# Kernel optimization log

Measured on AMD Instinct MI355X. Metric: run time of the kernel, lower is better.

Reference implementation:

```python
import jax, jax.numpy as jnp
import numpy as np
from jax import lax


def _gru_layer(x_seq, W, U, b, units):
    """Keras GRU (reset_after=True, gate order [z, r, h]) with activation=relu.
    x_seq: (B, T, F). Returns (ys (B,T,units), h_last (B,units))."""
    b_in, b_rec = b[0], b[1]                      # each (3*units,)
    # Precompute all input projections once: (B, T, 3*units)
    x_proj = jnp.einsum('btf,fj->btj', x_seq, W) + b_in
    B = x_seq.shape[0]
    h0 = jnp.zeros((B, units), dtype=x_seq.dtype)

    def step(h, xp_t):
        rec = h @ U + b_rec                        # (B, 3*units)
        zr = jax.nn.sigmoid(xp_t[:, :2 * units] + rec[:, :2 * units])
        z, r = zr[:, :units], zr[:, units:]
        hh = jax.nn.relu(xp_t[:, 2 * units:] + r * rec[:, 2 * units:])
        h_new = z * h + (1.0 - z) * hh
        return h_new, h_new

    h_last, ys = lax.scan(step, h0, jnp.swapaxes(x_proj, 0, 1))  # scan over T
    return jnp.swapaxes(ys, 0, 1), h_last


def setup_inputs() -> dict:
    key = jax.random.key(0)
    ks = jax.random.split(key, 6)
    B, T, F, U1, U2 = 64, 2048, 15, 256, 256
    s = lambda fan_in: 1.0 / np.sqrt(fan_in)
    return {
        'input_data': jax.random.normal(ks[0], (B, T, F), dtype=jnp.float32),
        'W1': jax.random.normal(ks[1], (F, 3 * U1), dtype=jnp.float32) * s(F),
        'U1': jax.random.normal(ks[2], (U1, 3 * U1), dtype=jnp.float32) * s(U1),
        'b1': jnp.zeros((2, 3 * U1), dtype=jnp.float32),
        'W2': jax.random.normal(ks[3], (U1, 3 * U2), dtype=jnp.float32) * s(U1),
        'U2': jax.random.normal(ks[4], (U2, 3 * U2), dtype=jnp.float32) * s(U2),
        'b2': jnp.zeros((2, 3 * U2), dtype=jnp.float32),
    }


def reference(input_data, W1, U1, b1, W2, U2, b2):
    u1 = U1.shape[0]
    u2 = U2.shape[0]
    seq1, state1 = _gru_layer(input_data, W1, U1, b1, u1)  # gru1: return_sequences + state
    seq2, state2 = _gru_layer(seq1, W2, U2, b2, u2)        # gru2: last output + state
    x = seq2[:, -1, :]                                      # last output (== state2)
    return (x, state1, state2)
```

## Files before the change

kernel.cpp:

```cpp
#include <hip/hip_runtime.h>

#define BB 64
#define TT 2048
#define FF 15
#define UU 256
#define N3 768

typedef _Float16 half8 __attribute__((ext_vector_type(8)));
typedef float f32x4 __attribute__((ext_vector_type(4)));

__device__ float g_seq1[BB * TT * UU];
__device__ float g_xp[(size_t)BB * TT * N3];
__device__ uint4 g_U1p[48 * 8 * 64];
__device__ uint4 g_U2p[48 * 8 * 64];
__device__ uint4 g_W2p[48 * 8 * 64];

__global__ __launch_bounds__(256) void prep_upk(const float* __restrict__ U,
                                                unsigned* __restrict__ Up) {
    int idx = blockIdx.x * 256 + threadIdx.x;
    int d = idx & 3, l = (idx >> 2) & 63, kt = (idx >> 8) & 7, nt = idx >> 11;
    int row = kt * 32 + ((l >> 4) << 3) + 2 * d;
    int col = nt * 16 + (l & 15);
    unsigned short lo = __builtin_bit_cast(unsigned short, (_Float16)U[row * N3 + col]);
    unsigned short hi = __builtin_bit_cast(unsigned short, (_Float16)U[(row + 1) * N3 + col]);
    Up[idx] = (unsigned)lo | ((unsigned)hi << 16);
}

__global__ __launch_bounds__(256) void gemm_k15(
    const float* __restrict__ x, const float* __restrict__ W1,
    const float* __restrict__ bin, float* __restrict__ C) {
    __shared__ float xr[8][FF];
    const int m0 = blockIdx.x * 8;
    const int j  = blockIdx.y * 256 + threadIdx.x;
    if (threadIdx.x < 8 * FF) {
        int r = threadIdx.x / FF, k = threadIdx.x - r * FF;
        xr[r][k] = x[(size_t)(m0 + r) * FF + k];
    }
    __syncthreads();
    float wv[FF];
#pragma unroll
    for (int k = 0; k < FF; k++) wv[k] = W1[k * N3 + j];
    const float bj = bin[j];
#pragma unroll
    for (int r = 0; r < 8; r++) {
        float a = bj;
#pragma unroll
        for (int k = 0; k < FF; k++) a += xr[r][k] * wv[k];
        C[(size_t)(m0 + r) * N3 + j] = a;
    }
}

__global__ __launch_bounds__(512) void gemm_xp_mfma(
    const float* __restrict__ A, const uint4* __restrict__ Wp,
    const float* __restrict__ bin, float* __restrict__ C) {
    const int tid = threadIdx.x, w = tid >> 6, lane = tid & 63;
    const int mt = w >> 1;
    const int nb = (w & 1) * 24;
    const int arow = blockIdx.x * 64 + mt * 16 + (lane & 15);
    const int ko   = (lane >> 4) * 8;

    f32x4 acc[24] = {};
    const float* ap = A + (size_t)arow * 256 + ko;

#pragma unroll
    for (int kt = 0; kt < 8; kt++) {
        float4 p0 = *(const float4*)(ap + kt * 32);
        float4 p1 = *(const float4*)(ap + kt * 32 + 4);
        half8 av;
        av[0] = (_Float16)p0.x; av[1] = (_Float16)p0.y;
        av[2] = (_Float16)p0.z; av[3] = (_Float16)p0.w;
        av[4] = (_Float16)p1.x; av[5] = (_Float16)p1.y;
        av[6] = (_Float16)p1.z; av[7] = (_Float16)p1.w;
        const uint4* wp = Wp + (size_t)(nb * 8 + kt) * 64 + lane;
#pragma unroll
        for (int n = 0; n < 24; n++) {
            half8 bf = __builtin_bit_cast(half8, wp[(size_t)n * 8 * 64]);
            acc[n] = __builtin_amdgcn_mfma_f32_16x16x32_f16(av, bf, acc[n], 0, 0, 0);
        }
    }
    const int rbase = blockIdx.x * 64 + mt * 16 + (lane >> 4) * 4;
#pragma unroll
    for (int n = 0; n < 24; n++) {
        int col = (nb + n) * 16 + (lane & 15);
        float bv = bin[col];
#pragma unroll
        for (int d = 0; d < 4; d++)
            C[(size_t)(rbase + d) * N3 + col] = acc[n][d] + bv;
    }
}

__global__ __launch_bounds__(512) __attribute__((amdgpu_waves_per_eu(2, 2)))
void gru_mfma2(const uint4* __restrict__ Up, const float* __restrict__ brec,
               const float* __restrict__ xp, float* __restrict__ seq_out,
               float* __restrict__ state_out, float* __restrict__ extra_out) {
    const int b = blockIdx.x, tid = threadIdx.x;
    const int w = tid >> 6, lane = tid & 63;
    const int l15 = lane & 15;
    const int uA = 32 * w + l15, uB = uA + 16;

    __shared__ __align__(16) _Float16 h2s[2][UU];

    const int tz = 2 * w, tr = 16 + 2 * w, th = 32 + 2 * w;
    half8 ub[48];
#pragma unroll
    for (int kt = 0; kt < 8; kt++) {
        ub[0 * 8 + kt] = __builtin_bit_cast(half8, Up[((tz + 0) * 8 + kt) * 64 + lane]);
        ub[1 * 8 + kt] = __builtin_bit_cast(half8, Up[((tz + 1) * 8 + kt) * 64 + lane]);
        ub[2 * 8 + kt] = __builtin_bit_cast(half8, Up[((tr + 0) * 8 + kt) * 64 + lane]);
        ub[3 * 8 + kt] = __builtin_bit_cast(half8, Up[((tr + 1) * 8 + kt) * 64 + lane]);
        ub[4 * 8 + kt] = __builtin_bit_cast(half8, Up[((th + 0) * 8 + kt) * 64 + lane]);
        ub[5 * 8 + kt] = __builtin_bit_cast(half8, Up[((th + 1) * 8 + kt) * 64 + lane]);
    }
    const float brzA = brec[uA], brrA = brec[uA + UU], brhA = brec[uA + 2 * UU];
    const float brzB = brec[uB], brrB = brec[uB + UU], brhB = brec[uB + 2 * UU];

    if (tid < 128) ((unsigned*)h2s[0])[tid] = 0u;
    float hA = 0.f, hB = 0.f;
    __syncthreads();

    const float* __restrict__ xpb = xp + (size_t)b * TT * N3;
    float xzA = xpb[uA], xrA = xpb[uA + UU], xhA = xpb[uA + 2 * UU];
    float xzB = xpb[uB], xrB = xpb[uB + UU], xhB = xpb[uB + 2 * UU];

    const int arow = (lane >> 4) << 3;

    for (int t = 0; t < TT; t++) {
        const float* xn = xpb + (size_t)(t + 1 < TT ? t + 1 : t) * N3;
        float xzAn = xn[uA], xrAn = xn[uA + UU], xhAn = xn[uA + 2 * UU];
        float xzBn = xn[uB], xrBn = xn[uB + UU], xhBn = xn[uB + 2 * UU];

        const _Float16* hcur = h2s[t & 1];
        f32x4 a0 = {0.f, 0.f, 0.f, 0.f}, a1 = a0, a2 = a0, a3 = a0, a4 = a0, a5 = a0;
#pragma unroll
        for (int kt = 0; kt < 8; kt++) {
            half8 av = *(const half8*)&hcur[kt * 32 + arow];
            a0 = __builtin_amdgcn_mfma_f32_16x16x32_f16(av, ub[0 * 8 + kt], a0, 0, 0, 0);
            a1 = __builtin_amdgcn_mfma_f32_16x16x32_f16(av, ub[1 * 8 + kt], a1, 0, 0, 0);
            a2 = __builtin_amdgcn_mfma_f32_16x16x32_f16(av, ub[2 * 8 + kt], a2, 0, 0, 0);
            a3 = __builtin_amdgcn_mfma_f32_16x16x32_f16(av, ub[3 * 8 + kt], a3, 0, 0, 0);
            a4 = __builtin_amdgcn_mfma_f32_16x16x32_f16(av, ub[4 * 8 + kt], a4, 0, 0, 0);
            a5 = __builtin_amdgcn_mfma_f32_16x16x32_f16(av, ub[5 * 8 + kt], a5, 0, 0, 0);
        }

        float zA = 1.f / (1.f + __expf(-(xzA + a0[0] + brzA)));
        float zB = 1.f / (1.f + __expf(-(xzB + a1[0] + brzB)));
        float rA = 1.f / (1.f + __expf(-(xrA + a2[0] + brrA)));
        float rB = 1.f / (1.f + __expf(-(xrB + a3[0] + brrB)));
        float hhA = xhA + rA * (a4[0] + brhA); hhA = hhA > 0.f ? hhA : 0.f;
        float hhB = xhB + rB * (a5[0] + brhB); hhB = hhB > 0.f ? hhB : 0.f;
        hA = zA * hA + (1.f - zA) * hhA;
        hB = zB * hB + (1.f - zB) * hhB;

        _Float16* hnxt = h2s[(t + 1) & 1];
        if (lane < 32) {
            int   u  = (lane < 16) ? uA : uB;
            float hv = (lane < 16) ? hA : hB;
            hnxt[u] = (_Float16)hv;
            if (seq_out)
                seq_out[(size_t)b * TT * UU + (size_t)t * UU + u] = hv;
        }
        __syncthreads();
        xzA = xzAn; xrA = xrAn; xhA = xhAn;
        xzB = xzBn; xrB = xrBn; xhB = xhBn;
    }

    if (lane < 32) {
        int   u  = (lane < 16) ? uA : uB;
        float hv = (lane < 16) ? hA : hB;
        state_out[b * UU + u] = hv;
        if (extra_out) extra_out[b * UU + u] = hv;
    }
}

extern "C" void kernel_launch(void* const* d_in, const int* in_sizes, int n_in,
                              void* d_out, int out_size, void* d_ws, size_t ws_size,
                              hipStream_t stream) {
    const float* x  = (const float*)d_in[0];
    const float* W1 = (const float*)d_in[1];
    const float* U1 = (const float*)d_in[2];
    const float* b1 = (const float*)d_in[3];
    const float* W2 = (const float*)d_in[4];
    const float* U2 = (const float*)d_in[5];
    const float* b2 = (const float*)d_in[6];
    float* out = (float*)d_out;

    uint4* U1p; hipGetSymbolAddress((void**)&U1p, HIP_SYMBOL(g_U1p));
    uint4* U2p; hipGetSymbolAddress((void**)&U2p, HIP_SYMBOL(g_U2p));
    uint4* W2p; hipGetSymbolAddress((void**)&W2p, HIP_SYMBOL(g_W2p));
    float* seq1; hipGetSymbolAddress((void**)&seq1, HIP_SYMBOL(g_seq1));
    float* xp;   hipGetSymbolAddress((void**)&xp,   HIP_SYMBOL(g_xp));

    prep_upk<<<384, 256, 0, stream>>>(U1, (unsigned*)U1p);
    prep_upk<<<384, 256, 0, stream>>>(U2, (unsigned*)U2p);
    prep_upk<<<384, 256, 0, stream>>>(W2, (unsigned*)W2p);

    gemm_k15<<<dim3(BB * TT / 8, 3), 256, 0, stream>>>(x, W1, b1, xp);
    gru_mfma2<<<BB, 512, 0, stream>>>(U1p, b1 + N3, xp, seq1, out + BB * UU, nullptr);

    gemm_xp_mfma<<<BB * TT / 64, 512, 0, stream>>>(seq1, W2p, b2, xp);
    gru_mfma2<<<BB, 512, 0, stream>>>(U2p, b2 + N3, xp, nullptr, out + 2 * BB * UU, out);
}
```

Measured before the change: 5.026 ms.

## Store seq1 and input projections in fp16 and reorder recurrent MFMAs

The intermediate buffers for the layer-1 output sequence and the input projections now hold fp16 instead of fp32. This halves the HBM traffic of the projection GEMMs and of the per-step xp loads in the recurrent kernels. The recurrent step also preloads all eight h fragments from shared memory before issuing the MFMAs, and computes the r/h gate chains ahead of the z gate so that the dependent math can start sooner. The cost is extra rounding of the projections and of seq1, which may reduce accuracy over the 2048 steps.

```diff
diff --git a/kernel.cpp b/kernel.cpp
--- a/kernel.cpp
+++ b/kernel.cpp
@@ -9,8 +9,8 @@
 typedef _Float16 half8 __attribute__((ext_vector_type(8)));
 typedef float f32x4 __attribute__((ext_vector_type(4)));
 
-__device__ float g_seq1[BB * TT * UU];
-__device__ float g_xp[(size_t)BB * TT * N3];
+__device__ _Float16 g_seq1[BB * TT * UU];
+__device__ _Float16 g_xp[(size_t)BB * TT * N3];
 __device__ uint4 g_U1p[48 * 8 * 64];
 __device__ uint4 g_U2p[48 * 8 * 64];
 __device__ uint4 g_W2p[48 * 8 * 64];
@@ -28,7 +28,7 @@
 
 __global__ __launch_bounds__(256) void gemm_k15(
     const float* __restrict__ x, const float* __restrict__ W1,
-    const float* __restrict__ bin, float* __restrict__ C) {
+    const float* __restrict__ bin, _Float16* __restrict__ C) {
     __shared__ float xr[8][FF];
     const int m0 = blockIdx.x * 8;
     const int j  = blockIdx.y * 256 + threadIdx.x;
@@ -46,13 +46,13 @@
         float a = bj;
 #pragma unroll
         for (int k = 0; k < FF; k++) a += xr[r][k] * wv[k];
-        C[(size_t)(m0 + r) * N3 + j] = a;
+        C[(size_t)(m0 + r) * N3 + j] = (_Float16)a;
     }
 }
 
 __global__ __launch_bounds__(512) void gemm_xp_mfma(
-    const float* __restrict__ A, const uint4* __restrict__ Wp,
-    const float* __restrict__ bin, float* __restrict__ C) {
+    const _Float16* __restrict__ A, const uint4* __restrict__ Wp,
+    const float* __restrict__ bin, _Float16* __restrict__ C) {
     const int tid = threadIdx.x, w = tid >> 6, lane = tid & 63;
     const int mt = w >> 1;
     const int nb = (w & 1) * 24;
@@ -60,17 +60,11 @@
     const int ko   = (lane >> 4) * 8;
 
     f32x4 acc[24] = {};
-    const float* ap = A + (size_t)arow * 256 + ko;
+    const _Float16* ap = A + (size_t)arow * 256 + ko;
 
 #pragma unroll
     for (int kt = 0; kt < 8; kt++) {
-        float4 p0 = *(const float4*)(ap + kt * 32);
-        float4 p1 = *(const float4*)(ap + kt * 32 + 4);
-        half8 av;
-        av[0] = (_Float16)p0.x; av[1] = (_Float16)p0.y;
-        av[2] = (_Float16)p0.z; av[3] = (_Float16)p0.w;
-        av[4] = (_Float16)p1.x; av[5] = (_Float16)p1.y;
-        av[6] = (_Float16)p1.z; av[7] = (_Float16)p1.w;
+        half8 av = *(const half8*)(ap + kt * 32);
         const uint4* wp = Wp + (size_t)(nb * 8 + kt) * 64 + lane;
 #pragma unroll
         for (int n = 0; n < 24; n++) {
@@ -85,13 +79,13 @@
         float bv = bin[col];
 #pragma unroll
         for (int d = 0; d < 4; d++)
-            C[(size_t)(rbase + d) * N3 + col] = acc[n][d] + bv;
+            C[(size_t)(rbase + d) * N3 + col] = (_Float16)(acc[n][d] + bv);
     }
 }
 
 __global__ __launch_bounds__(512) __attribute__((amdgpu_waves_per_eu(2, 2)))
 void gru_mfma2(const uint4* __restrict__ Up, const float* __restrict__ brec,
-               const float* __restrict__ xp, float* __restrict__ seq_out,
+               const _Float16* __restrict__ xp, _Float16* __restrict__ seq_out,
                float* __restrict__ state_out, float* __restrict__ extra_out) {
     const int b = blockIdx.x, tid = threadIdx.x;
     const int w = tid >> 6, lane = tid & 63;
@@ -118,36 +112,46 @@
     float hA = 0.f, hB = 0.f;
     __syncthreads();
 
-    const float* __restrict__ xpb = xp + (size_t)b * TT * N3;
-    float xzA = xpb[uA], xrA = xpb[uA + UU], xhA = xpb[uA + 2 * UU];
-    float xzB = xpb[uB], xrB = xpb[uB + UU], xhB = xpb[uB + 2 * UU];
+    const _Float16* __restrict__ xpb = xp + (size_t)b * TT * N3;
+    float xzA = (float)xpb[uA], xrA = (float)xpb[uA + UU], xhA = (float)xpb[uA + 2 * UU];
+    float xzB = (float)xpb[uB], xrB = (float)xpb[uB + UU], xhB = (float)xpb[uB + 2 * UU];
 
     const int arow = (lane >> 4) << 3;
+    const f32x4 kZ = {0.f, 0.f, 0.f, 0.f};
 
     for (int t = 0; t < TT; t++) {
-        const float* xn = xpb + (size_t)(t + 1 < TT ? t + 1 : t) * N3;
-        float xzAn = xn[uA], xrAn = xn[uA + UU], xhAn = xn[uA + 2 * UU];
-        float xzBn = xn[uB], xrBn = xn[uB + UU], xhBn = xn[uB + 2 * UU];
+        const _Float16* xn = xpb + (size_t)(t + 1 < TT ? t + 1 : t) * N3;
+        float xzAn = (float)xn[uA], xrAn = (float)xn[uA + UU], xhAn = (float)xn[uA + 2 * UU];
+        float xzBn = (float)xn[uB], xrBn = (float)xn[uB + UU], xhBn = (float)xn[uB + 2 * UU];
 
         const _Float16* hcur = h2s[t & 1];
-        f32x4 a0 = {0.f, 0.f, 0.f, 0.f}, a1 = a0, a2 = a0, a3 = a0, a4 = a0, a5 = a0;
-#pragma unroll
-        for (int kt = 0; kt < 8; kt++) {
-            half8 av = *(const half8*)&hcur[kt * 32 + arow];
-            a0 = __builtin_amdgcn_mfma_f32_16x16x32_f16(av, ub[0 * 8 + kt], a0, 0, 0, 0);
-            a1 = __builtin_amdgcn_mfma_f32_16x16x32_f16(av, ub[1 * 8 + kt], a1, 0, 0, 0);
-            a2 = __builtin_amdgcn_mfma_f32_16x16x32_f16(av, ub[2 * 8 + kt], a2, 0, 0, 0);
-            a3 = __builtin_amdgcn_mfma_f32_16x16x32_f16(av, ub[3 * 8 + kt], a3, 0, 0, 0);
-            a4 = __builtin_amdgcn_mfma_f32_16x16x32_f16(av, ub[4 * 8 + kt], a4, 0, 0, 0);
-            a5 = __builtin_amdgcn_mfma_f32_16x16x32_f16(av, ub[5 * 8 + kt], a5, 0, 0, 0);
+        half8 av[8];
+#pragma unroll
+        for (int kt = 0; kt < 8; kt++)
+            av[kt] = *(const half8*)&hcur[kt * 32 + arow];
+
+        f32x4 a2 = __builtin_amdgcn_mfma_f32_16x16x32_f16(av[0], ub[2 * 8], kZ, 0, 0, 0);
+        f32x4 a3 = __builtin_amdgcn_mfma_f32_16x16x32_f16(av[0], ub[3 * 8], kZ, 0, 0, 0);
+        f32x4 a4 = __builtin_amdgcn_mfma_f32_16x16x32_f16(av[0], ub[4 * 8], kZ, 0, 0, 0);
+        f32x4 a5 = __builtin_amdgcn_mfma_f32_16x16x32_f16(av[0], ub[5 * 8], kZ, 0, 0, 0);
+        f32x4 a0 = __builtin_amdgcn_mfma_f32_16x16x32_f16(av[0], ub[0 * 8], kZ, 0, 0, 0);
+        f32x4 a1 = __builtin_amdgcn_mfma_f32_16x16x32_f16(av[0], ub[1 * 8], kZ, 0, 0, 0);
+#pragma unroll
+        for (int kt = 1; kt < 8; kt++) {
+            a2 = __builtin_amdgcn_mfma_f32_16x16x32_f16(av[kt], ub[2 * 8 + kt], a2, 0, 0, 0);
+            a3 = __builtin_amdgcn_mfma_f32_16x16x32_f16(av[kt], ub[3 * 8 + kt], a3, 0, 0, 0);
+            a4 = __builtin_amdgcn_mfma_f32_16x16x32_f16(av[kt], ub[4 * 8 + kt], a4, 0, 0, 0);
+            a5 = __builtin_amdgcn_mfma_f32_16x16x32_f16(av[kt], ub[5 * 8 + kt], a5, 0, 0, 0);
+            a0 = __builtin_amdgcn_mfma_f32_16x16x32_f16(av[kt], ub[0 * 8 + kt], a0, 0, 0, 0);
+            a1 = __builtin_amdgcn_mfma_f32_16x16x32_f16(av[kt], ub[1 * 8 + kt], a1, 0, 0, 0);
         }
 
-        float zA = 1.f / (1.f + __expf(-(xzA + a0[0] + brzA)));
-        float zB = 1.f / (1.f + __expf(-(xzB + a1[0] + brzB)));
         float rA = 1.f / (1.f + __expf(-(xrA + a2[0] + brrA)));
         float rB = 1.f / (1.f + __expf(-(xrB + a3[0] + brrB)));
         float hhA = xhA + rA * (a4[0] + brhA); hhA = hhA > 0.f ? hhA : 0.f;
         float hhB = xhB + rB * (a5[0] + brhB); hhB = hhB > 0.f ? hhB : 0.f;
+        float zA = 1.f / (1.f + __expf(-(xzA + a0[0] + brzA)));
+        float zB = 1.f / (1.f + __expf(-(xzB + a1[0] + brzB)));
         hA = zA * hA + (1.f - zA) * hhA;
         hB = zB * hB + (1.f - zB) * hhB;
 
@@ -155,9 +159,10 @@
         if (lane < 32) {
             int   u  = (lane < 16) ? uA : uB;
             float hv = (lane < 16) ? hA : hB;
-            hnxt[u] = (_Float16)hv;
+            _Float16 hq = (_Float16)hv;
+            hnxt[u] = hq;
             if (seq_out)
-                seq_out[(size_t)b * TT * UU + (size_t)t * UU + u] = hv;
+                seq_out[(size_t)b * TT * UU + (size_t)t * UU + u] = hq;
         }
         __syncthreads();
         xzA = xzAn; xrA = xrAn; xhA = xhAn;
@@ -187,8 +192,8 @@
     uint4* U1p; hipGetSymbolAddress((void**)&U1p, HIP_SYMBOL(g_U1p));
     uint4* U2p; hipGetSymbolAddress((void**)&U2p, HIP_SYMBOL(g_U2p));
     uint4* W2p; hipGetSymbolAddress((void**)&W2p, HIP_SYMBOL(g_W2p));
-    float* seq1; hipGetSymbolAddress((void**)&seq1, HIP_SYMBOL(g_seq1));
-    float* xp;   hipGetSymbolAddress((void**)&xp,   HIP_SYMBOL(g_xp));
+    _Float16* seq1; hipGetSymbolAddress((void**)&seq1, HIP_SYMBOL(g_seq1));
+    _Float16* xp;   hipGetSymbolAddress((void**)&xp,   HIP_SYMBOL(g_xp));
 
     prep_upk<<<384, 256, 0, stream>>>(U1, (unsigned*)U1p);
     prep_upk<<<384, 256, 0, stream>>>(U2, (unsigned*)U2p);
```

After: 5.525 ms. 9.9% more time.
